# Kernel optimization log

Measured on AMD Instinct MI355X. Metric: run time of the kernel, lower is better.

## Reference

```python
import jax, jax.numpy as jnp
import numpy as np

L, D, H = 5, 300, 600          # num_layers, emb_dim, mlp hidden (2*emb_dim)
NG = 512                       # number of graphs in the batch
ATOM_V, BOND_V = 64, 8         # per-feature vocab sizes
BN_EPS = 1e-5


def _bn(h, gamma, beta):
    # BatchNorm1d in training mode (batch statistics, biased variance)
    mu = h.mean(axis=0)
    var = ((h - mu) ** 2).mean(axis=0)
    return (h - mu) * jax.lax.rsqrt(var + BN_EPS) * gamma + beta


def reference(x, edge_index, edge_attr, batch,
              atom_emb, bond_emb, eps, W1, b1, g1, be1, W2, b2, g2, be2,
              head_w, head_b):
    N = x.shape[0]
    # AtomEncoder: sum of per-feature embeddings, feature f uses rows [f*ATOM_V, (f+1)*ATOM_V)
    h = atom_emb[x + jnp.arange(x.shape[1]) * ATOM_V].sum(axis=1)          # [N, D]
    e_idx = edge_attr + jnp.arange(edge_attr.shape[1]) * BOND_V            # [E, 3]
    src, dst = edge_index[0], edge_index[1]
    for l in range(L):
        e = bond_emb[l][e_idx].sum(axis=1)                                 # per-layer BondEncoder [E, D]
        msg = jax.nn.relu(h[src] + e)                                      # gather + message [E, D]
        agg = jax.ops.segment_sum(msg, dst, num_segments=N)                # scatter-add [N, D]
        z = (1.0 + eps[l]) * h + agg                                       # GIN update
        z = jax.nn.relu(_bn(z @ W1[l] + b1[l], g1[l], be1[l]))             # mlp: Lin+BN+ReLU
        z = z @ W2[l] + b2[l]                                              # mlp: Lin
        h = _bn(z, g2[l], be2[l])                                          # outer BatchNorm
        if l < L - 1:                                                      # no ReLU on last layer
            h = jax.nn.relu(h)
    hg = jax.ops.segment_sum(h, batch, num_segments=NG)                    # global_add_pool [NG, D]
    mu = hg.mean(axis=1, keepdims=True)                                    # GroupNorm(1, D, affine=False)
    var = ((hg - mu) ** 2).mean(axis=1, keepdims=True)
    hg = (hg - mu) * jax.lax.rsqrt(var + BN_EPS)
    return hg @ head_w + head_b                                            # [NG, num_tasks]


def setup_inputs() -> dict:
    key = jax.random.key(0)
    ks = jax.random.split(key, 12)
    N, E = 20000, 320000
    x = jax.random.randint(ks[0], (N, 9), 0, ATOM_V)
    edge_index = jax.random.randint(ks[1], (2, E), 0, N)
    edge_attr = jax.random.randint(ks[2], (E, 3), 0, BOND_V)
    batch = jnp.sort(jax.random.randint(ks[3], (N,), 0, NG))
    f = lambda k, shp: jax.random.normal(k, shp, dtype=jnp.float32) * 0.02
    return dict(
        x=x, edge_index=edge_index, edge_attr=edge_attr, batch=batch,
        atom_emb=f(ks[4], (9 * ATOM_V, D)),
        bond_emb=f(ks[5], (L, 3 * BOND_V, D)),
        eps=jnp.zeros((L,), jnp.float32),
        W1=f(ks[6], (L, D, H)), b1=jnp.zeros((L, H), jnp.float32),
        g1=jnp.ones((L, H), jnp.float32), be1=jnp.zeros((L, H), jnp.float32),
        W2=f(ks[7], (L, H, D)), b2=jnp.zeros((L, D), jnp.float32),
        g2=jnp.ones((L, D), jnp.float32), be2=jnp.zeros((L, D), jnp.float32),
        head_w=f(ks[8], (D, 1)), head_b=jnp.zeros((1,), jnp.float32),
    )
```

## Files before the change

### kernel.cpp

```cpp
#include <hip/hip_runtime.h>
#include <cstddef>
#include <cstdint>

#define DD 300
#define HH 600
#define LL 5
#define NGG 512
#define KP1 320
#define KP2 608
#define NP1 640
#define NP2 384
#define Z2LD 304
#define CLD 304

typedef unsigned short u16;
typedef _Float16 f16x8 __attribute__((ext_vector_type(8)));
typedef _Float16 h2 __attribute__((ext_vector_type(2)));
typedef float f32x4 __attribute__((ext_vector_type(4)));

__device__ __forceinline__ u16 f2h(float v)
{
    _Float16 h = (_Float16)v; u16 u; __builtin_memcpy(&u, &h, 2); return u;
}
__device__ __forceinline__ float h2f(u16 u)
{
    _Float16 h; __builtin_memcpy(&h, &u, 2); return (float)h;
}

__device__ __forceinline__ void g2l16(const void* g, void* l)
{
    __builtin_amdgcn_global_load_lds(
        (const __attribute__((address_space(1))) void*)g,
        (__attribute__((address_space(3))) void*)l, 16, 0, 0);
}

__device__ __forceinline__ void bn_from_stats(float s, float q, float g, float be,
                                              float invn, float& sc, float& sh)
{
    float mu = s * invn;
    float var = q * invn - mu * mu;
    float rs = rsqrtf(var + 1e-5f);
    sc = rs * g;
    sh = be - mu * sc;
}

__global__ __launch_bounds__(320) void atom_combo(const int* __restrict__ x,
    const float* __restrict__ emb, const float* __restrict__ bond,
    u16* __restrict__ z2, u16* __restrict__ combo, int N)
{
    int b = blockIdx.x;
    int t = threadIdx.x;
    if (b < N) {
        __shared__ int xi[9];
        if (t < 9) xi[t] = x[b * 9 + t] + t * 64;
        __syncthreads();
        if (t >= Z2LD) return;
        if (t >= DD) { z2[(size_t)b * Z2LD + t] = 0; return; }
        float s = 0.f;
#pragma unroll
        for (int f = 0; f < 9; ++f) s += emb[(size_t)xi[f] * DD + t];
        z2[(size_t)b * Z2LD + t] = f2h(s);
    } else {
        int blk = b - N;
        int l = blk >> 9, code = blk & 511;
        if (t >= CLD) return;
        u16 val = 0;
        if (t < DD) {
            const float* bl = bond + (size_t)l * 24 * DD;
            float v = bl[(size_t)(code & 7) * DD + t]
                    + bl[(size_t)(8 + ((code >> 3) & 7)) * DD + t]
                    + bl[(size_t)(16 + (code >> 6)) * DD + t];
            val = f2h(v);
        }
        combo[(size_t)blk * CLD + t] = val;
    }
}

__global__ void csr_count(const int* __restrict__ dst, int E, int* __restrict__ cnt)
{
    int i = blockIdx.x * blockDim.x + threadIdx.x;
    int stride = gridDim.x * blockDim.x;
    for (; i < E; i += stride) atomicAdd(&cnt[dst[i]], 1);
}

__global__ __launch_bounds__(1024) void scan_kernel(const int* __restrict__ cnt,
    int* __restrict__ rowptr, int n)
{
    __shared__ int buf[1024];
    int t = threadIdx.x;
    int carry = 0;
    for (int base = 0; base < n; base += 1024) {
        int v = (base + t < n) ? cnt[base + t] : 0;
        buf[t] = v;
        __syncthreads();
        for (int off = 1; off < 1024; off <<= 1) {
            int x = (t >= off) ? buf[t - off] : 0;
            __syncthreads();
            buf[t] += x;
            __syncthreads();
        }
        if (base + t < n) rowptr[base + t] = buf[t] - v + carry;
        int total = buf[1023];
        __syncthreads();
        carry += total;
    }
    if (t == 0) rowptr[n] = carry;
}

__global__ void csr_fill(const int* __restrict__ src, const int* __restrict__ dst,
    const int* __restrict__ ea, const int* __restrict__ rowptr,
    int* __restrict__ cursor, int* __restrict__ rec, int E)
{
    int i = blockIdx.x * blockDim.x + threadIdx.x;
    int stride = gridDim.x * blockDim.x;
    for (; i < E; i += stride) {
        int d = dst[i];
        int pos = rowptr[d] + atomicAdd(&cursor[d], 1);
        int code = ea[i * 3] | (ea[i * 3 + 1] << 3) | (ea[i * 3 + 2] << 6);
        rec[pos] = src[i] | (code << 20);
    }
}

__global__ __launch_bounds__(256) void w_prep_t(const float* __restrict__ W,
    int K, int N, int KPp, int NPp, int ktiles, u16* __restrict__ Thi)
{
    __shared__ float tile[64][65];
    int ntiles = NPp >> 6;
    int blk = blockIdx.x;
    int l = blk / (ktiles * ntiles);
    int rem = blk % (ktiles * ntiles);
    int k0 = (rem / ntiles) << 6;
    int n0 = (rem % ntiles) << 6;
    int tn = threadIdx.x & 63;
    int tg = threadIdx.x >> 6;
    const float* Wl = W + (size_t)l * K * N;
    for (int kk = tg; kk < 64; kk += 4) {
        int gk = k0 + kk, gn = n0 + tn;
        tile[kk][tn] = (gk < K && gn < N) ? Wl[(size_t)gk * N + gn] : 0.f;
    }
    __syncthreads();
    for (int nn = tg; nn < 64; nn += 4) {
        int gn = n0 + nn, gk = k0 + tn;
        if (gk < KPp) {
            size_t o = ((size_t)l * NPp + gn) * KPp + gk;
            Thi[o] = f2h(tile[tn][nn]);
        }
    }
}

template <bool AFF>
__global__ __launch_bounds__(256) void agg_kernel(const u16* __restrict__ z2,
    const int* __restrict__ rec, const int* __restrict__ rowptr,
    const u16* __restrict__ combo_l,
    const float* __restrict__ sc, const float* __restrict__ sh,
    const float* __restrict__ eps, int l, u16* __restrict__ A1)
{
    __shared__ float part[6][304];
    int n = blockIdx.x;
    int t = threadIdx.x;
    int eo = t / 38, ch = t - eo * 38;
    int d0 = ch * 8;
    int beg = rowptr[n], end = rowptr[n + 1];

    if (eo < 6) {
        float acc[8] = {0.f, 0.f, 0.f, 0.f, 0.f, 0.f, 0.f, 0.f};
        h2 scp[4], shp[4];
        const h2 zz = {(_Float16)0.f, (_Float16)0.f};
        if (AFF) {
#pragma unroll
            for (int j = 0; j < 4; ++j) {
                scp[j] = (h2){(_Float16)sc[d0 + 2 * j], (_Float16)sc[d0 + 2 * j + 1]};
                shp[j] = (h2){(_Float16)sh[d0 + 2 * j], (_Float16)sh[d0 + 2 * j + 1]};
            }
        }
        int i = beg + eo;
        for (; i + 6 < end; i += 12) {
            int r0 = rec[i], r1 = rec[i + 6];
            uint4 hv0 = *(const uint4*)(z2 + (size_t)(r0 & 0xFFFFF) * Z2LD + d0);
            uint4 cv0 = *(const uint4*)(combo_l + (size_t)(((unsigned)r0) >> 20) * CLD + d0);
            uint4 hv1 = *(const uint4*)(z2 + (size_t)(r1 & 0xFFFFF) * Z2LD + d0);
            uint4 cv1 = *(const uint4*)(combo_l + (size_t)(((unsigned)r1) >> 20) * CLD + d0);
            const h2* hp0 = (const h2*)&hv0; const h2* cp0 = (const h2*)&cv0;
            const h2* hp1 = (const h2*)&hv1; const h2* cp1 = (const h2*)&cv1;
#pragma unroll
            for (int j = 0; j < 4; ++j) {
                h2 a0 = hp0[j], a1 = hp1[j];
                if (AFF) {
                    a0 = __builtin_elementwise_max(a0 * scp[j] + shp[j], zz);
                    a1 = __builtin_elementwise_max(a1 * scp[j] + shp[j], zz);
                }
                h2 m0 = __builtin_elementwise_max(a0 + cp0[j], zz);
                h2 m1 = __builtin_elementwise_max(a1 + cp1[j], zz);
                acc[2 * j]     += (float)m0.x + (float)m1.x;
                acc[2 * j + 1] += (float)m0.y + (float)m1.y;
            }
        }
        for (; i < end; i += 6) {
            int r0 = rec[i];
            uint4 hv0 = *(const uint4*)(z2 + (size_t)(r0 & 0xFFFFF) * Z2LD + d0);
            uint4 cv0 = *(const uint4*)(combo_l + (size_t)(((unsigned)r0) >> 20) * CLD + d0);
            const h2* hp0 = (const h2*)&hv0; const h2* cp0 = (const h2*)&cv0;
#pragma unroll
            for (int j = 0; j < 4; ++j) {
                h2 a0 = hp0[j];
                if (AFF) a0 = __builtin_elementwise_max(a0 * scp[j] + shp[j], zz);
                h2 m0 = __builtin_elementwise_max(a0 + cp0[j], zz);
                acc[2 * j]     += (float)m0.x;
                acc[2 * j + 1] += (float)m0.y;
            }
        }
        *(float4*)&part[eo][d0]     = *(const float4*)&acc[0];
        *(float4*)&part[eo][d0 + 4] = *(const float4*)&acc[4];
    }
    __syncthreads();

    if (t < 152) {
        float se = 1.0f + eps[l];
        int d = t * 2;
#pragma unroll
        for (int k = 0; k < 2; ++k) {
            int dd = d + k;
            float s = part[0][dd] + part[1][dd] + part[2][dd]
                    + part[3][dd] + part[4][dd] + part[5][dd];
            float hn = h2f(z2[(size_t)n * Z2LD + dd]);
            if (AFF) hn = fmaxf(fmaf(hn, sc[dd], sh[dd]), 0.f);
            A1[(size_t)n * KP1 + dd] = f2h(fmaf(se, hn, s));
        }
    } else if (t < 160) {
        int d = 304 + (t - 152) * 2;
        A1[(size_t)n * KP1 + d] = 0;
        A1[(size_t)n * KP1 + d + 1] = 0;
    }
}

template <bool FUSE>
__global__ __launch_bounds__(512, 4) void gemm_rs(
    const u16* __restrict__ Af, int lda,
    const u16* __restrict__ Bw,
    const float* __restrict__ bias,
    const float* __restrict__ csA, const float* __restrict__ csqA,
    const float* __restrict__ gA, const float* __restrict__ beA, float invn,
    u16* __restrict__ O, int ldc, int M, int N, int ksteps,
    float* __restrict__ cs, float* __restrict__ csq, int ncol, int nwg)
{
    __shared__ __align__(16) u16 As[2][4][128][8];
    __shared__ __align__(16) u16 Bs[3][4][128][8];
    __shared__ float sc_s[FUSE ? 640 : 1], sh_s[FUSE ? 640 : 1];

    const int t = threadIdx.x;
    const int lane = t & 63, w = t >> 6;
    const int l15 = lane & 15, l4 = lane >> 4;
    const int wr = w >> 2, wc = w & 3;

    int orig = blockIdx.x;
    int q8 = nwg >> 3, r8 = nwg & 7;
    int xcd = orig & 7, i8 = orig >> 3;
    int wgid = (xcd < r8 ? xcd * (q8 + 1) : r8 * (q8 + 1) + (xcd - r8) * q8) + i8;
    const int col0 = (wgid % ncol) * 128;
    const int row0 = (wgid / ncol) * 128;

    if (FUSE) {
        for (int c = t; c < lda; c += 512) {
            float a = 0.f, b = 0.f;
            if (c < HH) bn_from_stats(csA[c], csqA[c], gA[c], beA[c], invn, a, b);
            sc_s[c] = a; sh_s[c] = b;
        }
    }

    const int arow = t >> 2;
    const int kg   = t & 3;
    const int k8   = kg * 8;
    const u16* aptr = Af + (size_t)(row0 + arow) * lda + k8;

    const int bkg = w >> 1, bch = w & 1;
    const u16* bptr = Bw + (size_t)(col0 + bch * 64 + lane) * lda + bkg * 8;

    auto loadAv = [&](int ks, uint4& pv) {
        pv = *(const uint4*)(aptr + ks * 32);
    };
    auto issueB = [&](int ks, int buf) {
        g2l16(bptr + ks * 32, &Bs[buf][bkg][bch * 64][0]);
    };
    auto writeAv = [&](int ks, int buf, uint4& pv) {
        if (FUSE) {
            const u16* hp = (const u16*)&pv;
            u16 oh[8];
#pragma unroll
            for (int j = 0; j < 8; ++j) {
                int c = ks * 32 + k8 + j;
                float xv = fmaxf(fmaf(h2f(hp[j]), sc_s[c], sh_s[c]), 0.f);
                oh[j] = f2h(xv);
            }
            *(uint4*)&As[buf][kg][arow][0] = *(const uint4*)oh;
        } else {
            *(uint4*)&As[buf][kg][arow][0] = pv;
        }
    };

    f32x4 acc[4][2];
#pragma unroll
    for (int i = 0; i < 4; ++i)
#pragma unroll
        for (int j = 0; j < 2; ++j) acc[i][j] = (f32x4){0.f, 0.f, 0.f, 0.f};

    uint4 pvA, pvB, pvC;
    __syncthreads();
    loadAv(0, pvA);
    issueB(0, 0);
    issueB(1, 1);
    loadAv(1, pvB);
    loadAv(2, pvC);
    writeAv(0, 0, pvA);
    asm volatile("s_waitcnt vmcnt(3) lgkmcnt(0)" ::: "memory");
    __builtin_amdgcn_s_barrier();

    int cur = 0, rb = 0, tb = 2;
    auto body = [&](int ks, uint4& hold, uint4& fill) {
        const bool more1 = (ks + 1 < ksteps), more2 = (ks + 2 < ksteps),
                   more3 = (ks + 3 < ksteps);
        if (more2) issueB(ks + 2, tb);
        if (more3) loadAv(ks + 3, fill);

        f16x8 a[4], b[2];
#pragma unroll
        for (int i = 0; i < 4; ++i) {
            int r = wr * 64 + i * 16 + l15;
            a[i] = *(const f16x8*)As[cur][l4][r];
        }
#pragma unroll
        for (int i = 0; i < 2; ++i) {
            int c = wc * 32 + i * 16 + l15;
            b[i] = *(const f16x8*)Bs[rb][l4][c];
        }
#pragma unroll
        for (int mi = 0; mi < 4; ++mi)
#pragma unroll
            for (int ni = 0; ni < 2; ++ni)
                acc[mi][ni] = __builtin_amdgcn_mfma_f32_16x16x32_f16(a[mi], b[ni], acc[mi][ni], 0, 0, 0);

        if (more1) {
            writeAv(ks + 1, cur ^ 1, hold);
            if (more3)      asm volatile("s_waitcnt vmcnt(3) lgkmcnt(0)" ::: "memory");
            else if (more2) asm volatile("s_waitcnt vmcnt(2) lgkmcnt(0)" ::: "memory");
            else            asm volatile("s_waitcnt vmcnt(0) lgkmcnt(0)" ::: "memory");
            __builtin_amdgcn_s_barrier();
        }
        cur ^= 1;
        rb = (rb == 2) ? 0 : rb + 1;
        tb = (tb == 2) ? 0 : tb + 1;
    };
    for (int k = 0; k < ksteps; k += 3) {
        body(k, pvB, pvA);
        if (k + 1 < ksteps) body(k + 1, pvC, pvB);
        if (k + 2 < ksteps) body(k + 2, pvA, pvC);
    }

    float colS[2] = {0.f, 0.f}, colQ[2] = {0.f, 0.f};
#pragma unroll
    for (int ni = 0; ni < 2; ++ni) {
        int gc = col0 + wc * 32 + ni * 16 + l15;
        float bb = (gc < N) ? bias[gc] : 0.f;
#pragma unroll
        for (int mi = 0; mi < 4; ++mi)
#pragma unroll
            for (int r = 0; r < 4; ++r) {
                int gr = row0 + wr * 64 + mi * 16 + l4 * 4 + r;
                if (gr >= M) continue;
                if (gc < N) {
                    float val = acc[mi][ni][r] + bb;
                    O[(size_t)gr * ldc + gc] = f2h(val);
                    colS[ni] += val;
                    colQ[ni] += val * val;
                } else if (gc < ldc) {
                    O[(size_t)gr * ldc + gc] = 0;
                }
            }
    }
#pragma unroll
    for (int ni = 0; ni < 2; ++ni) {
        float s = colS[ni], q = colQ[ni];
        s += __shfl_xor(s, 16); s += __shfl_xor(s, 32);
        q += __shfl_xor(q, 16); q += __shfl_xor(q, 32);
        int gc = col0 + wc * 32 + ni * 16 + l15;
        if (l4 == 0 && gc < N) {
            atomicAdd(&cs[gc], s);
            atomicAdd(&csq[gc], q);
        }
    }
}

__global__ void bn_fin(float* __restrict__ cs, float* __restrict__ csq,
                       const float* __restrict__ g, const float* __restrict__ be,
                       float* __restrict__ scale, float* __restrict__ shift,
                       int cols, int colspad, float invn,
                       float* __restrict__ extra, int nextra)
{
    int c = blockIdx.x * blockDim.x + threadIdx.x;
    if (c < nextra) { extra[c] = 0.f; extra[c + nextra] = 0.f; }
    if (c >= colspad) return;
    if (c >= cols) { scale[c] = 0.f; shift[c] = 0.f; return; }
    float mu = cs[c] * invn;
    float var = csq[c] * invn - mu * mu;
    float rs = rsqrtf(var + 1e-5f);
    float sc = rs * g[c];
    scale[c] = sc;
    shift[c] = be[c] - mu * sc;
    cs[c] = 0.f;
    csq[c] = 0.f;
}

__global__ __launch_bounds__(320) void pool_head(const u16* __restrict__ z2,
    const int* __restrict__ batch, int N,
    const float* __restrict__ sc, const float* __restrict__ sh,
    const float* __restrict__ w, const float* __restrict__ hb,
    float* __restrict__ out)
{
    __shared__ float red[320];
    int g = blockIdx.x;
    int t = threadIdx.x;
    int lo = 0, hi = N;
    while (lo < hi) { int mid = (lo + hi) >> 1; if (batch[mid] < g) lo = mid + 1; else hi = mid; }
    int start = lo;
    hi = N;
    while (lo < hi) { int mid = (lo + hi) >> 1; if (batch[mid] <= g) lo = mid + 1; else hi = mid; }
    int end = lo;

    float v = 0.f;
    if (t < DD) {
        float s = 0.f;
        for (int i = start; i < end; ++i) s += h2f(z2[(size_t)i * Z2LD + t]);
        v = sc[t] * s + (float)(end - start) * sh[t];
    }

    auto reduce = [&](float x) -> float {
        red[t] = x;
        __syncthreads();
        for (int off = 160; off >= 5; off >>= 1) {
            if (t < off) red[t] += red[t + off];
            __syncthreads();
        }
        float r = red[0] + red[1] + red[2] + red[3] + red[4];
        __syncthreads();
        return r;
    };

    float mean = reduce(v) * (1.f / (float)DD);
    float var  = reduce(v * v) * (1.f / (float)DD) - mean * mean;
    float rs = rsqrtf(var + 1e-5f);
    float contrib = (t < DD) ? (v - mean) * rs * w[t] : 0.f;
    float o = reduce(contrib);
    if (t == 0) out[g] = o + hb[0];
}

extern "C" void kernel_launch(void* const* d_in, const int* in_sizes, int n_in,
                              void* d_out, int out_size, void* d_ws, size_t ws_size,
                              hipStream_t stream)
{
    (void)n_in; (void)out_size; (void)ws_size;
    const int*   x         = (const int*)  d_in[0];
    const int*   edge_idx  = (const int*)  d_in[1];
    const int*   edge_attr = (const int*)  d_in[2];
    const int*   batch     = (const int*)  d_in[3];
    const float* atom_emb  = (const float*)d_in[4];
    const float* bond_emb  = (const float*)d_in[5];
    const float* eps       = (const float*)d_in[6];
    const float* W1        = (const float*)d_in[7];
    const float* b1        = (const float*)d_in[8];
    const float* g1        = (const float*)d_in[9];
    const float* be1       = (const float*)d_in[10];
    const float* W2        = (const float*)d_in[11];
    const float* b2        = (const float*)d_in[12];
    const float* g2        = (const float*)d_in[13];
    const float* be2       = (const float*)d_in[14];
    const float* head_w    = (const float*)d_in[15];
    const float* head_b    = (const float*)d_in[16];

    const int NN = in_sizes[3];
    const int E  = in_sizes[1] / 2;
    const int gm = (NN + 127) / 128;
    const int mpad = gm * 128;
    const float invn = 1.f / (float)NN;

    char* p = (char*)d_ws;
    auto alloc = [&](size_t bytes) { char* r = p; p += (bytes + 255) & ~(size_t)255; return r; };

    u16* z2g    = (u16*)  alloc((size_t)NN * Z2LD * 2);
    u16* A1     = (u16*)  alloc((size_t)mpad * KP1 * 2);
    u16* Z1     = (u16*)  alloc((size_t)mpad * KP2 * 2);
    u16* W1T    = (u16*)  alloc((size_t)LL * NP1 * KP1 * 2);
    u16* W2T    = (u16*)  alloc((size_t)LL * NP2 * KP2 * 2);
    u16* combo  = (u16*)  alloc((size_t)LL * 512 * CLD * 2);
    float* stats = (float*)alloc((608 * 2 + 304 * 2) * 4);
    float* cs1  = stats;
    float* csq1 = cs1 + 608;
    float* cs2  = csq1 + 608;
    float* csq2 = cs2 + 304;
    float* sc2  = (float*)alloc(Z2LD * 4);
    float* sh2  = (float*)alloc(Z2LD * 4);
    int* cnt    = (int*)  alloc((size_t)NN * 4 * 2);
    int* cursor = cnt + NN;
    int* rowptr = (int*)  alloc((size_t)(NN + 1) * 4);
    int* rec    = (int*)  alloc((size_t)E * 4);

    const int* src = edge_idx;
    const int* dst = edge_idx + E;

    hipMemsetAsync(cnt, 0, (size_t)NN * 2 * sizeof(int), stream);
    hipMemsetAsync(stats, 0, (608 * 2 + 304 * 2) * sizeof(float), stream);
    csr_count<<<512, 256, 0, stream>>>(dst, E, cnt);
    scan_kernel<<<1, 1024, 0, stream>>>(cnt, rowptr, NN);
    csr_fill<<<512, 256, 0, stream>>>(src, dst, edge_attr, rowptr, cursor, rec, E);
    w_prep_t<<<LL * (KP1 / 64) * (NP1 / 64), 256, 0, stream>>>(
        W1, DD, HH, KP1, NP1, KP1 / 64, W1T);
    w_prep_t<<<LL * ((KP2 + 63) / 64) * (NP2 / 64), 256, 0, stream>>>(
        W2, HH, DD, KP2, NP2, (KP2 + 63) / 64, W2T);
    atom_combo<<<NN + LL * 512, 320, 0, stream>>>(x, atom_emb, bond_emb, z2g, combo, NN);

    const int nwg1 = (NP1 / 128) * gm;
    const int nwg2 = (NP2 / 128) * gm;
    for (int l = 0; l < LL; ++l) {
        const u16* combo_l = combo + (size_t)l * 512 * CLD;
        if (l == 0)
            agg_kernel<false><<<NN, 256, 0, stream>>>(z2g, rec, rowptr, combo_l,
                nullptr, nullptr, eps, l, A1);
        else
            agg_kernel<true><<<NN, 256, 0, stream>>>(z2g, rec, rowptr, combo_l,
                sc2, sh2, eps, l, A1);

        gemm_rs<false><<<nwg1, 512, 0, stream>>>(
            A1, KP1, W1T + (size_t)l * NP1 * KP1,
            b1 + (size_t)l * HH, nullptr, nullptr, nullptr, nullptr, invn,
            Z1, KP2, NN, HH, KP1 / 32, cs1, csq1, NP1 / 128, nwg1);

        gemm_rs<true><<<nwg2, 512, 0, stream>>>(
            Z1, KP2, W2T + (size_t)l * NP2 * KP2,
            b2 + (size_t)l * DD,
            cs1, csq1, g1 + (size_t)l * HH, be1 + (size_t)l * HH, invn,
            z2g, Z2LD, NN, DD, KP2 / 32, cs2, csq2, NP2 / 128, nwg2);

        bn_fin<<<3, 256, 0, stream>>>(cs2, csq2, g2 + (size_t)l * DD,
            be2 + (size_t)l * DD, sc2, sh2, DD, Z2LD, invn, cs1, 608);
    }

    pool_head<<<NGG, 320, 0, stream>>>(z2g, batch, NN, sc2, sh2, head_w, head_b,
                                       (float*)d_out);
}
```

Before: 642.3 us.

## Double GEMM M-tile to 256 rows per workgroup for B-tile reuse

Templates the GEMM on a row multiplier and launches both MLP GEMMs with 256-row tiles, so each thread loads two A rows and each warp computes eight M-fragments. Each B tile staged in LDS is now reused across twice as many rows, which halves weight traffic and workgroup count. In exchange register pressure and LDS use go up, launch bounds drop to 2 waves per EU, and the grid shrinks to about 395 and 237 workgroups on 256 CUs, which lowers occupancy and can leave CUs poorly balanced. The wait counts are adjusted for the extra outstanding loads.

```diff
diff --git a/kernel.cpp b/kernel.cpp
--- a/kernel.cpp
+++ b/kernel.cpp
@@ -233,8 +233,8 @@
     }
 }
 
-template <bool FUSE>
-__global__ __launch_bounds__(512, 4) void gemm_rs(
+template <bool FUSE, int RM>
+__global__ __launch_bounds__(512, 2) void gemm_rs(
     const u16* __restrict__ Af, int lda,
     const u16* __restrict__ Bw,
     const float* __restrict__ bias,
@@ -243,7 +243,7 @@
     u16* __restrict__ O, int ldc, int M, int N, int ksteps,
     float* __restrict__ cs, float* __restrict__ csq, int ncol, int nwg)
 {
-    __shared__ __align__(16) u16 As[2][4][128][8];
+    __shared__ __align__(16) u16 As[2][4][128 * RM][8];
     __shared__ __align__(16) u16 Bs[3][4][128][8];
     __shared__ float sc_s[FUSE ? 640 : 1], sh_s[FUSE ? 640 : 1];
 
@@ -257,7 +257,7 @@
     int xcd = orig & 7, i8 = orig >> 3;
     int wgid = (xcd < r8 ? xcd * (q8 + 1) : r8 * (q8 + 1) + (xcd - r8) * q8) + i8;
     const int col0 = (wgid % ncol) * 128;
-    const int row0 = (wgid / ncol) * 128;
+    const int row0 = (wgid / ncol) * (128 * RM);
 
     if (FUSE) {
         for (int c = t; c < lda; c += 512) {
@@ -275,35 +275,40 @@
     const int bkg = w >> 1, bch = w & 1;
     const u16* bptr = Bw + (size_t)(col0 + bch * 64 + lane) * lda + bkg * 8;
 
-    auto loadAv = [&](int ks, uint4& pv) {
-        pv = *(const uint4*)(aptr + ks * 32);
+    auto loadAv = [&](int ks, uint4 (&pv)[RM]) {
+#pragma unroll
+        for (int rr = 0; rr < RM; ++rr)
+            pv[rr] = *(const uint4*)(aptr + (size_t)rr * 128 * lda + ks * 32);
     };
     auto issueB = [&](int ks, int buf) {
         g2l16(bptr + ks * 32, &Bs[buf][bkg][bch * 64][0]);
     };
-    auto writeAv = [&](int ks, int buf, uint4& pv) {
-        if (FUSE) {
-            const u16* hp = (const u16*)&pv;
-            u16 oh[8];
-#pragma unroll
-            for (int j = 0; j < 8; ++j) {
-                int c = ks * 32 + k8 + j;
-                float xv = fmaxf(fmaf(h2f(hp[j]), sc_s[c], sh_s[c]), 0.f);
-                oh[j] = f2h(xv);
+    auto writeAv = [&](int ks, int buf, uint4 (&pv)[RM]) {
+#pragma unroll
+        for (int rr = 0; rr < RM; ++rr) {
+            if (FUSE) {
+                const u16* hp = (const u16*)&pv[rr];
+                u16 oh[8];
+#pragma unroll
+                for (int j = 0; j < 8; ++j) {
+                    int c = ks * 32 + k8 + j;
+                    float xv = fmaxf(fmaf(h2f(hp[j]), sc_s[c], sh_s[c]), 0.f);
+                    oh[j] = f2h(xv);
+                }
+                *(uint4*)&As[buf][kg][rr * 128 + arow][0] = *(const uint4*)oh;
+            } else {
+                *(uint4*)&As[buf][kg][rr * 128 + arow][0] = pv[rr];
             }
-            *(uint4*)&As[buf][kg][arow][0] = *(const uint4*)oh;
-        } else {
-            *(uint4*)&As[buf][kg][arow][0] = pv;
         }
     };
 
-    f32x4 acc[4][2];
-#pragma unroll
-    for (int i = 0; i < 4; ++i)
+    f32x4 acc[4 * RM][2];
+#pragma unroll
+    for (int i = 0; i < 4 * RM; ++i)
 #pragma unroll
         for (int j = 0; j < 2; ++j) acc[i][j] = (f32x4){0.f, 0.f, 0.f, 0.f};
 
-    uint4 pvA, pvB, pvC;
+    uint4 pvA[RM], pvB[RM], pvC[RM];
     __syncthreads();
     loadAv(0, pvA);
     issueB(0, 0);
@@ -311,20 +316,21 @@
     loadAv(1, pvB);
     loadAv(2, pvC);
     writeAv(0, 0, pvA);
-    asm volatile("s_waitcnt vmcnt(3) lgkmcnt(0)" ::: "memory");
+    if constexpr (RM == 2) asm volatile("s_waitcnt vmcnt(5) lgkmcnt(0)" ::: "memory");
+    else                   asm volatile("s_waitcnt vmcnt(3) lgkmcnt(0)" ::: "memory");
     __builtin_amdgcn_s_barrier();
 
     int cur = 0, rb = 0, tb = 2;
-    auto body = [&](int ks, uint4& hold, uint4& fill) {
+    auto body = [&](int ks, uint4 (&hold)[RM], uint4 (&fill)[RM]) {
         const bool more1 = (ks + 1 < ksteps), more2 = (ks + 2 < ksteps),
                    more3 = (ks + 3 < ksteps);
         if (more2) issueB(ks + 2, tb);
         if (more3) loadAv(ks + 3, fill);
 
-        f16x8 a[4], b[2];
-#pragma unroll
-        for (int i = 0; i < 4; ++i) {
-            int r = wr * 64 + i * 16 + l15;
+        f16x8 a[4 * RM], b[2];
+#pragma unroll
+        for (int i = 0; i < 4 * RM; ++i) {
+            int r = wr * (64 * RM) + i * 16 + l15;
             a[i] = *(const f16x8*)As[cur][l4][r];
         }
 #pragma unroll
@@ -333,16 +339,22 @@
             b[i] = *(const f16x8*)Bs[rb][l4][c];
         }
 #pragma unroll
-        for (int mi = 0; mi < 4; ++mi)
+        for (int mi = 0; mi < 4 * RM; ++mi)
 #pragma unroll
             for (int ni = 0; ni < 2; ++ni)
                 acc[mi][ni] = __builtin_amdgcn_mfma_f32_16x16x32_f16(a[mi], b[ni], acc[mi][ni], 0, 0, 0);
 
         if (more1) {
             writeAv(ks + 1, cur ^ 1, hold);
-            if (more3)      asm volatile("s_waitcnt vmcnt(3) lgkmcnt(0)" ::: "memory");
-            else if (more2) asm volatile("s_waitcnt vmcnt(2) lgkmcnt(0)" ::: "memory");
-            else            asm volatile("s_waitcnt vmcnt(0) lgkmcnt(0)" ::: "memory");
+            if (more3) {
+                if constexpr (RM == 2) asm volatile("s_waitcnt vmcnt(5) lgkmcnt(0)" ::: "memory");
+                else                   asm volatile("s_waitcnt vmcnt(3) lgkmcnt(0)" ::: "memory");
+            } else if (more2) {
+                if constexpr (RM == 2) asm volatile("s_waitcnt vmcnt(3) lgkmcnt(0)" ::: "memory");
+                else                   asm volatile("s_waitcnt vmcnt(2) lgkmcnt(0)" ::: "memory");
+            } else {
+                asm volatile("s_waitcnt vmcnt(0) lgkmcnt(0)" ::: "memory");
+            }
             __builtin_amdgcn_s_barrier();
         }
         cur ^= 1;
@@ -361,10 +373,10 @@
         int gc = col0 + wc * 32 + ni * 16 + l15;
         float bb = (gc < N) ? bias[gc] : 0.f;
 #pragma unroll
-        for (int mi = 0; mi < 4; ++mi)
+        for (int mi = 0; mi < 4 * RM; ++mi)
 #pragma unroll
             for (int r = 0; r < 4; ++r) {
-                int gr = row0 + wr * 64 + mi * 16 + l4 * 4 + r;
+                int gr = row0 + wr * (64 * RM) + mi * 16 + l4 * 4 + r;
                 if (gr >= M) continue;
                 if (gc < N) {
                     float val = acc[mi][ni][r] + bb;
@@ -477,8 +489,8 @@
 
     const int NN = in_sizes[3];
     const int E  = in_sizes[1] / 2;
-    const int gm = (NN + 127) / 128;
-    const int mpad = gm * 128;
+    const int rows256 = (NN + 255) / 256;
+    const int mpad = rows256 * 256;
     const float invn = 1.f / (float)NN;
 
     char* p = (char*)d_ws;
@@ -516,8 +528,8 @@
         W2, HH, DD, KP2, NP2, (KP2 + 63) / 64, W2T);
     atom_combo<<<NN + LL * 512, 320, 0, stream>>>(x, atom_emb, bond_emb, z2g, combo, NN);
 
-    const int nwg1 = (NP1 / 128) * gm;
-    const int nwg2 = (NP2 / 128) * gm;
+    const int nwg1 = (NP1 / 128) * rows256;
+    const int nwg2 = (NP2 / 128) * rows256;
     for (int l = 0; l < LL; ++l) {
         const u16* combo_l = combo + (size_t)l * 512 * CLD;
         if (l == 0)
@@ -527,12 +539,12 @@
             agg_kernel<true><<<NN, 256, 0, stream>>>(z2g, rec, rowptr, combo_l,
                 sc2, sh2, eps, l, A1);
 
-        gemm_rs<false><<<nwg1, 512, 0, stream>>>(
+        gemm_rs<false, 2><<<nwg1, 512, 0, stream>>>(
             A1, KP1, W1T + (size_t)l * NP1 * KP1,
             b1 + (size_t)l * HH, nullptr, nullptr, nullptr, nullptr, invn,
             Z1, KP2, NN, HH, KP1 / 32, cs1, csq1, NP1 / 128, nwg1);
 
-        gemm_rs<true><<<nwg2, 512, 0, stream>>>(
+        gemm_rs<true, 2><<<nwg2, 512, 0, stream>>>(
             Z1, KP2, W2T + (size_t)l * NP2 * KP2,
             b2 + (size_t)l * DD,
             cs1, csq1, g1 + (size_t)l * HH, be1 + (size_t)l * HH, invn,
```

Result: slower. 757.7 us (+18.0%).
